# Kernel optimization log

Hardware: AMD Instinct MI355X
Metric: run time of the kernel (lower is better)

## Reference

```python
import jax, jax.numpy as jnp
import numpy as np

B, C, H, W = 4, 64, 96, 96
KS, NH = 7, 4


def setup_inputs() -> dict:
    key = jax.random.key(0)
    ks = jax.random.split(key, 9)
    s = 0.1  # keep logits in a sane range for softmax
    return {
        "input_x": jax.random.normal(ks[0], (B, C, H, W), jnp.float32),
        "q_w": jax.random.normal(ks[1], (C, C), jnp.float32) * s,
        "q_b": jax.random.normal(ks[2], (C,), jnp.float32) * s,
        "k_w": jax.random.normal(ks[3], (C, C), jnp.float32) * s,
        "k_b": jax.random.normal(ks[4], (C,), jnp.float32) * s,
        "v_w": jax.random.normal(ks[5], (C, C), jnp.float32) * s,
        "v_b": jax.random.normal(ks[6], (C,), jnp.float32) * s,
        "rel_h": jax.random.normal(ks[7], (C // 2, KS, 1), jnp.float32) * s,
        "rel_w": jax.random.normal(ks[8], (C // 2, 1, KS), jnp.float32) * s,
    }


def _unfold(x, ks):
    # x: (B, C, Hp, Wp) -> (B, C, Ho, Wo, ks, ks), same as torch .unfold(2).unfold(3)
    Hp, Wp = x.shape[2], x.shape[3]
    Ho, Wo = Hp - ks + 1, Wp - ks + 1
    ih = jnp.arange(Ho)[:, None] + jnp.arange(ks)[None, :]  # (Ho, ks)
    iw = jnp.arange(Wo)[:, None] + jnp.arange(ks)[None, :]  # (Wo, ks)
    return x[:, :, ih[:, None, :, None], iw[None, :, None, :]]


def reference(input_x, q_w, q_b, k_w, k_b, v_w, v_b, rel_h, rel_w):
    b, c, h, w = input_x.shape
    ks, nh = KS, NH
    dkh = c // nh
    p0 = (ks - 1) // 2
    p1 = ks - 1 - p0
    padded = jnp.pad(input_x, ((0, 0), (0, 0), (p0, p1), (p0, p1)))

    conv1x1 = lambda x, wt, bi: jnp.einsum('bchw,oc->bohw', x, wt) + bi[None, :, None, None]
    k = conv1x1(padded, k_w, k_b)
    v = conv1x1(padded, v_w, v_b)
    q = conv1x1(input_x, q_w, q_b)

    # flat reshapes exactly as in torch (row-major), reproducing its layout semantics
    k = _unfold(k, ks).reshape(b, nh, h, w, dkh, ks * ks)
    v = _unfold(v, ks).reshape(b, nh, h, w, dkh, ks * ks)
    q = q.reshape(b, nh, h, w, dkh)  # torch: (b,nh,h,w,dkh,1) squeezed

    qk = jnp.einsum('bnxyd,bnxydk->bnxyk', q, k).reshape(b, nh, h, w, ks, ks)
    # torch einsum 'bhxydz,cij->bhxyij' == (sum_d q) outer (sum_c rel)
    qsum = q.sum(-1)  # (b, nh, h, w)
    rel = rel_h.sum(0) + rel_w.sum(0)  # broadcasts to (ks, ks)
    qk = qk + qsum[..., None, None] * rel

    weights = jax.nn.softmax(qk.reshape(b, nh, h, w, ks * ks), axis=-1)
    attn = jnp.einsum('bnxyk,bnxydk->bnxyd', weights, v)  # (b, nh, h, w, dkh)
    attn = attn.reshape(b, c, h, w)  # flat reshape, matching torch
    return jax.nn.relu(attn)
```

## Files before the change

### kernel.cpp

```cpp
#include <hip/hip_runtime.h>

#define B_ 4
#define C_ 64
#define H_ 96
#define W_ 96
#define KS_ 7
#define NPIX (H_ * W_)
#define PR_ 102
#define PC_ 104
#define PSLAB (PR_ * PC_)
#define LDK 108

typedef __attribute__((ext_vector_type(8))) short short8;
typedef __attribute__((ext_vector_type(4))) float f32x4;

static __device__ inline ushort f2bf(float f) {
    union { float f; unsigned u; } v; v.f = f;
    unsigned r = (v.u + 0x7fff + ((v.u >> 16) & 1)) >> 16;
    return (ushort)r;
}


__global__ __launch_bounds__(256) void mfma_conv_kernel(
    const float* __restrict__ in,
    const float* __restrict__ qw, const float* __restrict__ qb,
    const float* __restrict__ kw, const float* __restrict__ kb,
    const float* __restrict__ vw, const float* __restrict__ vb,
    const float* __restrict__ relh, const float* __restrict__ relw,
    float* __restrict__ qf, float* __restrict__ kvf, float* __restrict__ rel_out)
{
    const int b    = blockIdx.y;
    const int pix0 = blockIdx.x * 32;
    const int t    = threadIdx.x;
    const int lane = t & 63;
    const int wv   = t >> 6;

    if (blockIdx.x == 0 && b == 0 && t < 49) {
        const int i = t / KS_, j = t % KS_;
        float s = 0.f;
        #pragma unroll
        for (int cc = 0; cc < C_ / 2; ++cc)
            s += relh[cc * KS_ + i] + relw[cc * KS_ + j];
        rel_out[t] = s;
    }

    {
        const int base = blockIdx.x * 256 + t;
        #pragma unroll
        for (int rep = 0; rep < 3; ++rep) {
            const int idx = base + rep * 73728;
            if (idx < 153600) {
                const int cell   = idx % 1200;
                const int chh    = (idx / 1200) & 63;
                const int tensor = idx / 76800;
                int pr, pw;
                if (cell < 312)      { pr = cell / PC_;              pw = cell % PC_; }
                else if (cell < 624) { int j2 = cell - 312; pr = 99 + j2 / PC_; pw = j2 % PC_; }
                else                 { int j2 = cell - 624; pr = 3 + j2 / 6; int s2 = j2 % 6;
                                       pw = (s2 < 3) ? s2 : 96 + s2; }
                const float bias = (tensor ? vb : kb)[chh];
                kvf[((size_t)(b * 2 + tensor) * C_ + chh) * PSLAB + pr * PC_ + pw] = bias;
            }
        }
    }

    __shared__ ushort xs[32 * 64];

    {
        const int pix = t & 31, cg = t >> 5;
        const float* xp = in + (size_t)b * C_ * NPIX + pix0 + pix;
        #pragma unroll
        for (int g = 0; g < 2; ++g) {
            const int ch = (cg + 8 * g) * 4;
            float x0 = xp[(size_t)(ch    ) * NPIX];
            float x1 = xp[(size_t)(ch + 1) * NPIX];
            float x2 = xp[(size_t)(ch + 2) * NPIX];
            float x3 = xp[(size_t)(ch + 3) * NPIX];
            ushort4 u = make_ushort4(f2bf(x0), f2bf(x1), f2bf(x2), f2bf(x3));
            unsigned byte = (unsigned)(pix * 128 + ch * 2) ^ (unsigned)((pix & 7) << 4);
            *reinterpret_cast<ushort4*>(reinterpret_cast<char*>(xs) + byte) = u;
        }
    }

    short8 afr[3][2];
    float  bi[3][4];
    #pragma unroll
    for (int i = 0; i < 3; ++i) {
        const int mt  = 3 * wv + i;
        const int row = mt * 16 + (lane & 15);
        const float* wsrc = (mt < 4) ? qw + row * 64
                          : (mt < 8) ? kw + (row - 64) * 64
                                     : vw + (row - 128) * 64;
        #pragma unroll
        for (int ka = 0; ka < 2; ++ka) {
            const int kk = ka * 32 + (lane >> 4) * 8;
            float4 a = *reinterpret_cast<const float4*>(wsrc + kk);
            float4 c = *reinterpret_cast<const float4*>(wsrc + kk + 4);
            short8 s;
            s[0] = (short)f2bf(a.x); s[1] = (short)f2bf(a.y);
            s[2] = (short)f2bf(a.z); s[3] = (short)f2bf(a.w);
            s[4] = (short)f2bf(c.x); s[5] = (short)f2bf(c.y);
            s[6] = (short)f2bf(c.z); s[7] = (short)f2bf(c.w);
            afr[i][ka] = s;
        }
        const int brow = mt * 16 + (lane >> 4) * 4;
        const float* bsrc = (mt < 4) ? qb + brow
                          : (mt < 8) ? kb + (brow - 64)
                                     : vb + (brow - 128);
        #pragma unroll
        for (int r = 0; r < 4; ++r) bi[i][r] = bsrc[r];
    }
    __syncthreads();

    short8 bfr[2][2];
    #pragma unroll
    for (int nt = 0; nt < 2; ++nt) {
        const int pl = nt * 16 + (lane & 15);
        #pragma unroll
        for (int ka = 0; ka < 2; ++ka) {
            const int kk = ka * 32 + (lane >> 4) * 8;
            unsigned byte = (unsigned)(pl * 128 + kk * 2) ^ (unsigned)((pl & 7) << 4);
            bfr[nt][ka] = *reinterpret_cast<const short8*>(
                reinterpret_cast<const char*>(xs) + byte);
        }
    }
    f32x4 acc[3][2];
    #pragma unroll
    for (int i = 0; i < 3; ++i) {
        f32x4 bv;
        #pragma unroll
        for (int r = 0; r < 4; ++r) bv[r] = bi[i][r];
        #pragma unroll
        for (int nt = 0; nt < 2; ++nt) acc[i][nt] = bv;
    }
    #pragma unroll
    for (int i = 0; i < 3; ++i) {
        #pragma unroll
        for (int nt = 0; nt < 2; ++nt) {
            acc[i][nt] = __builtin_amdgcn_mfma_f32_16x16x32_bf16(
                afr[i][0], bfr[nt][0], acc[i][nt], 0, 0, 0);
            acc[i][nt] = __builtin_amdgcn_mfma_f32_16x16x32_bf16(
                afr[i][1], bfr[nt][1], acc[i][nt], 0, 0, 0);
        }
    }
    #pragma unroll
    for (int i = 0; i < 3; ++i) {
        const int mt = 3 * wv + i;
        #pragma unroll
        for (int nt = 0; nt < 2; ++nt) {
            const int pix = pix0 + nt * 16 + (lane & 15);
            const int h = pix / 96, w = pix - h * 96;
            #pragma unroll
            for (int r = 0; r < 4; ++r) {
                const int row = mt * 16 + (lane >> 4) * 4 + r;
                if (mt < 4) {
                    qf[((size_t)b * C_ + row) * NPIX + pix] = acc[i][nt][r];
                } else {
                    const int tensor = (mt < 8) ? 0 : 1;
                    const int ch = (mt & 3) * 16 + (lane >> 4) * 4 + r;
                    kvf[((size_t)(b * 2 + tensor) * C_ + ch) * PSLAB
                        + (h + 3) * PC_ + (w + 3)] = acc[i][nt][r];
                }
            }
        }
    }
}

__global__ __launch_bounds__(192) void attn_kernel(
    const float* __restrict__ qf, const float* __restrict__ kvf,
    const float* __restrict__ rel, float* __restrict__ out)
{
    const int bx   = blockIdx.x;
    const int tile = bx % 3;
    const int c    = (bx / 3) % C_;
    const int b    = bx / (3 * C_);
    const int ho0  = tile * 32;
    const int t    = threadIdx.x;

    __shared__ __align__(16) float ksl[38 * LDK];
    __shared__ __align__(16) float vsl[38 * LDK];

    {
        const float* kbase = kvf + ((size_t)(b * 2 + 0) * C_ + c) * PSLAB + ho0 * PC_;
        const float* vbase = kvf + ((size_t)(b * 2 + 1) * C_ + c) * PSLAB + ho0 * PC_;
        #pragma unroll
        for (int s0 = 0; s0 < 6; ++s0) {
            const int idx = t + s0 * 192;
            if (idx < 988) {
                const int rl = idx / 26, c4 = (idx - rl * 26) * 4;
                *reinterpret_cast<float4*>(&ksl[rl * LDK + c4]) =
                    *reinterpret_cast<const float4*>(kbase + rl * PC_ + c4);
                *reinterpret_cast<float4*>(&vsl[rl * LDK + c4]) =
                    *reinterpret_cast<const float4*>(vbase + rl * PC_ + c4);
            }
        }
    }
    __syncthreads();

    const int r0 = t / 6;
    const int w0 = (t % 6) * 16;
    const int ho = ho0 + r0;

    const float LOG2E = 1.44269504f;
    const float* qp = qf + ((size_t)b * C_ + c) * NPIX + ho * W_ + w0;
    float qs[16];
    #pragma unroll
    for (int tt = 0; tt < 16; tt += 4) {
        float4 f = *reinterpret_cast<const float4*>(qp + tt);
        qs[tt] = f.x * LOG2E; qs[tt + 1] = f.y * LOG2E;
        qs[tt + 2] = f.z * LOG2E; qs[tt + 3] = f.w * LOG2E;
    }
    float qsum = 0.f;
    #pragma unroll
    for (int tt = 0; tt < 16; ++tt) qsum += qs[tt];

    float p[49];
    #pragma unroll
    for (int i = 0; i < KS_; ++i) {
        float kr[24];
        const float* kp = &ksl[(r0 + i) * LDK + w0];
        #pragma unroll
        for (int tt = 0; tt < 24; tt += 4) {
            float4 f = *reinterpret_cast<const float4*>(kp + tt);
            kr[tt] = f.x; kr[tt + 1] = f.y; kr[tt + 2] = f.z; kr[tt + 3] = f.w;
        }
        #pragma unroll
        for (int j = 0; j < KS_; ++j) {
            float s0 = 0.f, s1 = 0.f, s2 = 0.f, s3 = 0.f;
            #pragma unroll
            for (int tt = 0; tt < 16; tt += 4) {
                s0 = fmaf(qs[tt],     kr[tt + j],     s0);
                s1 = fmaf(qs[tt + 1], kr[tt + 1 + j], s1);
                s2 = fmaf(qs[tt + 2], kr[tt + 2 + j], s2);
                s3 = fmaf(qs[tt + 3], kr[tt + 3 + j], s3);
            }
            p[i * KS_ + j] = (s0 + s1) + (s2 + s3) + qsum * rel[i * KS_ + j];
        }
    }

    float m0 = p[0], m1 = p[1], m2 = p[2], m3 = p[3];
    #pragma unroll
    for (int kk = 4; kk < 48; kk += 4) {
        m0 = fmaxf(m0, p[kk]);     m1 = fmaxf(m1, p[kk + 1]);
        m2 = fmaxf(m2, p[kk + 2]); m3 = fmaxf(m3, p[kk + 3]);
    }
    float m = fmaxf(fmaxf(fmaxf(m0, m1), fmaxf(m2, m3)), p[48]);

    float e0 = 0.f, e1 = 0.f, e2 = 0.f, e3 = 0.f;
    #pragma unroll
    for (int kk = 0; kk < 48; kk += 4) {
        float a0 = exp2f(p[kk]     - m);
        float a1 = exp2f(p[kk + 1] - m);
        float a2 = exp2f(p[kk + 2] - m);
        float a3 = exp2f(p[kk + 3] - m);
        p[kk] = a0; p[kk + 1] = a1; p[kk + 2] = a2; p[kk + 3] = a3;
        e0 += a0; e1 += a1; e2 += a2; e3 += a3;
    }
    float a48 = exp2f(p[48] - m);
    p[48] = a48;
    const float inv = 1.f / ((e0 + e1) + (e2 + e3) + a48);

    float o16[16];
    #pragma unroll
    for (int d = 0; d < 16; ++d) o16[d] = 0.f;

    #pragma unroll
    for (int i = 0; i < KS_; ++i) {
        float vf[24];
        const float* vp = &vsl[(r0 + i) * LDK + w0];
        #pragma unroll
        for (int tt = 0; tt < 24; tt += 4) {
            float4 f = *reinterpret_cast<const float4*>(vp + tt);
            vf[tt] = f.x; vf[tt + 1] = f.y; vf[tt + 2] = f.z; vf[tt + 3] = f.w;
        }
        #pragma unroll
        for (int j = 0; j < KS_; ++j) {
            float wgt = p[i * KS_ + j];
            #pragma unroll
            for (int d = 0; d < 16; ++d) o16[d] = fmaf(wgt, vf[d + j], o16[d]);
        }
    }

    float* op = out + (((size_t)b * C_ + c) * H_ + ho) * W_ + w0;
    #pragma unroll
    for (int d = 0; d < 16; d += 4) {
        float4 f;
        f.x = fmaxf(o16[d]     * inv, 0.f);
        f.y = fmaxf(o16[d + 1] * inv, 0.f);
        f.z = fmaxf(o16[d + 2] * inv, 0.f);
        f.w = fmaxf(o16[d + 3] * inv, 0.f);
        *reinterpret_cast<float4*>(op + d) = f;
    }
}

extern "C" void kernel_launch(void* const* d_in, const int* in_sizes, int n_in,
                              void* d_out, int out_size, void* d_ws, size_t ws_size,
                              hipStream_t stream) {
    const float* in   = (const float*)d_in[0];
    const float* qw   = (const float*)d_in[1];
    const float* qb   = (const float*)d_in[2];
    const float* kw   = (const float*)d_in[3];
    const float* kb   = (const float*)d_in[4];
    const float* vw   = (const float*)d_in[5];
    const float* vb   = (const float*)d_in[6];
    const float* relh = (const float*)d_in[7];
    const float* relw = (const float*)d_in[8];
    float* out = (float*)d_out;

    float* qf  = (float*)d_ws;
    float* kvf = qf + (size_t)B_ * C_ * NPIX;
    float* rel = kvf + (size_t)B_ * 2 * C_ * PSLAB;

    dim3 cgrid(NPIX / 32, B_);
    mfma_conv_kernel<<<cgrid, 256, 0, stream>>>(in, qw, qb, kw, kb, vw, vb,
                                                relh, relw, qf, kvf, rel);

    dim3 agrid(B_ * C_ * 3);
    attn_kernel<<<agrid, 192, 0, stream>>>(qf, kvf, rel, out);
}
```

Measured before the change: 37.64 us.

## Stage conv outputs through LDS for float4 stores and shift padded column offset

The conv kernel now writes its MFMA accumulators into a shared-memory tile, synchronises, and then emits coalesced float4 stores to the q and padded k/v buffers, replacing scattered scalar stores. The padded slab's left pad is widened from 3 to 4 columns so that interior rows start 16-byte aligned, and the border-fill indexing and the attention kernel's K/V column reads shift by one to match. Occupancy hints are added to both kernels' launch bounds. This adds about 25 KB of LDS per block and one barrier in the conv kernel, and the attention kernel's 24-float row reads must still cover the extra column offset.

```diff
diff --git a/kernel.cpp b/kernel.cpp
--- a/kernel.cpp
+++ b/kernel.cpp
@@ -10,6 +10,7 @@
 #define PC_ 104
 #define PSLAB (PR_ * PC_)
 #define LDK 108
+#define CSTR 33
 
 typedef __attribute__((ext_vector_type(8))) short short8;
 typedef __attribute__((ext_vector_type(4))) float f32x4;
@@ -21,7 +22,7 @@
 }
 
 
-__global__ __launch_bounds__(256) void mfma_conv_kernel(
+__global__ __launch_bounds__(256, 4) void mfma_conv_kernel(
     const float* __restrict__ in,
     const float* __restrict__ qw, const float* __restrict__ qb,
     const float* __restrict__ kw, const float* __restrict__ kb,
@@ -49,15 +50,15 @@
         #pragma unroll
         for (int rep = 0; rep < 3; ++rep) {
             const int idx = base + rep * 73728;
-            if (idx < 153600) {
-                const int cell   = idx % 1200;
-                const int chh    = (idx / 1200) & 63;
-                const int tensor = idx / 76800;
+            if (idx < 178176) {
+                const int cell   = idx % 1392;
+                const int chh    = (idx / 1392) & 63;
+                const int tensor = idx / 89088;
                 int pr, pw;
                 if (cell < 312)      { pr = cell / PC_;              pw = cell % PC_; }
                 else if (cell < 624) { int j2 = cell - 312; pr = 99 + j2 / PC_; pw = j2 % PC_; }
-                else                 { int j2 = cell - 624; pr = 3 + j2 / 6; int s2 = j2 % 6;
-                                       pw = (s2 < 3) ? s2 : 96 + s2; }
+                else                 { int j2 = cell - 624; pr = 3 + j2 / 8; int s2 = j2 & 7;
+                                       pw = (s2 < 4) ? s2 : 96 + s2 - 4 + 4; }
                 const float bias = (tensor ? vb : kb)[chh];
                 kvf[((size_t)(b * 2 + tensor) * C_ + chh) * PSLAB + pr * PC_ + pw] = bias;
             }
@@ -65,6 +66,7 @@
     }
 
     __shared__ ushort xs[32 * 64];
+    __shared__ float  cs[192 * CSTR];
 
     {
         const int pix = t & 31, cg = t >> 5;
@@ -143,30 +145,41 @@
                 afr[i][1], bfr[nt][1], acc[i][nt], 0, 0, 0);
         }
     }
+
     #pragma unroll
     for (int i = 0; i < 3; ++i) {
-        const int mt = 3 * wv + i;
         #pragma unroll
         for (int nt = 0; nt < 2; ++nt) {
-            const int pix = pix0 + nt * 16 + (lane & 15);
-            const int h = pix / 96, w = pix - h * 96;
             #pragma unroll
             for (int r = 0; r < 4; ++r) {
-                const int row = mt * 16 + (lane >> 4) * 4 + r;
-                if (mt < 4) {
-                    qf[((size_t)b * C_ + row) * NPIX + pix] = acc[i][nt][r];
-                } else {
-                    const int tensor = (mt < 8) ? 0 : 1;
-                    const int ch = (mt & 3) * 16 + (lane >> 4) * 4 + r;
-                    kvf[((size_t)(b * 2 + tensor) * C_ + ch) * PSLAB
-                        + (h + 3) * PC_ + (w + 3)] = acc[i][nt][r];
-                }
+                const int row = (3 * wv + i) * 16 + (lane >> 4) * 4 + r;
+                cs[row * CSTR + nt * 16 + (lane & 15)] = acc[i][nt][r];
             }
         }
     }
+    __syncthreads();
+    #pragma unroll
+    for (int s = 0; s < 6; ++s) {
+        const int chunk = t + 256 * s;
+        const int row = chunk >> 3;
+        const int c4  = (chunk & 7) * 4;
+        float4 val = make_float4(cs[row * CSTR + c4],     cs[row * CSTR + c4 + 1],
+                                 cs[row * CSTR + c4 + 2], cs[row * CSTR + c4 + 3]);
+        const int pix = pix0 + c4;
+        if (row < 64) {
+            *reinterpret_cast<float4*>(&qf[((size_t)b * C_ + row) * NPIX + pix]) = val;
+        } else {
+            const int tensor = (row >= 128) ? 1 : 0;
+            const int ch = row & 63;
+            const int h = pix / 96, w = pix - h * 96;
+            *reinterpret_cast<float4*>(
+                &kvf[((size_t)(b * 2 + tensor) * C_ + ch) * PSLAB
+                     + (h + 3) * PC_ + (w + 4)]) = val;
+        }
+    }
 }
 
-__global__ __launch_bounds__(192) void attn_kernel(
+__global__ __launch_bounds__(192, 3) void attn_kernel(
     const float* __restrict__ qf, const float* __restrict__ kvf,
     const float* __restrict__ rel, float* __restrict__ out)
 {
@@ -229,10 +242,10 @@
             float s0 = 0.f, s1 = 0.f, s2 = 0.f, s3 = 0.f;
             #pragma unroll
             for (int tt = 0; tt < 16; tt += 4) {
-                s0 = fmaf(qs[tt],     kr[tt + j],     s0);
-                s1 = fmaf(qs[tt + 1], kr[tt + 1 + j], s1);
-                s2 = fmaf(qs[tt + 2], kr[tt + 2 + j], s2);
-                s3 = fmaf(qs[tt + 3], kr[tt + 3 + j], s3);
+                s0 = fmaf(qs[tt],     kr[1 + tt + j],     s0);
+                s1 = fmaf(qs[tt + 1], kr[1 + tt + 1 + j], s1);
+                s2 = fmaf(qs[tt + 2], kr[1 + tt + 2 + j], s2);
+                s3 = fmaf(qs[tt + 3], kr[1 + tt + 3 + j], s3);
             }
             p[i * KS_ + j] = (s0 + s1) + (s2 + s3) + qsum * rel[i * KS_ + j];
         }
@@ -277,7 +290,7 @@
         for (int j = 0; j < KS_; ++j) {
             float wgt = p[i * KS_ + j];
             #pragma unroll
-            for (int d = 0; d < 16; ++d) o16[d] = fmaf(wgt, vf[d + j], o16[d]);
+            for (int d = 0; d < 16; ++d) o16[d] = fmaf(wgt, vf[1 + d + j], o16[d]);
         }
     }
 
```

Result: slower. 42.46 us (+12.8%).
